# Optimization experiments

Hardware: AMD Instinct MI355X
Metric: run time of the kernel (lower is better)

Reference implementation:

```python
import jax, jax.numpy as jnp
from jax import lax
import numpy as np

B, T, D = 8, 512, 512
TS = 2 * T          # skip length = upsampled length
DI, DS, DTR, K, NL = 2 * D, 16, 32, 4, 2  # d_inner, d_state, dt_rank, d_conv, n_layers


def setup_inputs() -> dict:
    key = jax.random.key(0)
    ks = jax.random.split(key, 12)
    f = lambda k, s: jax.random.normal(k, s, dtype=jnp.float32)
    sc = 0.02
    A_log = jnp.log(jnp.arange(1, DS + 1, dtype=jnp.float32))  # S4D-real init
    A_log = jnp.tile(A_log[None, None, :], (NL, DI, 1))
    return {
        "x": f(ks[0], (B, T, D)),
        "skip": f(ks[1], (B, TS, D)),
        "up_w": f(ks[2], (D, D, K)) * sc,        # torch ConvTranspose1d weight (in,out,k)
        "up_b": jnp.zeros((D,), jnp.float32),
        "merge_w": f(ks[3], (D, 2 * D)) * sc,    # 1x1 conv (out,in)
        "merge_b": jnp.zeros((D,), jnp.float32),
        "ln_w": jnp.ones((D,), jnp.float32),
        "ln_b": jnp.zeros((D,), jnp.float32),
        "in_proj_w": f(ks[4], (NL, 2 * DI, D)) * sc,
        "conv_w": f(ks[5], (NL, DI, K)) * sc,    # depthwise causal conv
        "conv_b": jnp.zeros((NL, DI), jnp.float32),
        "x_proj_w": f(ks[6], (NL, DTR + 2 * DS, DI)) * sc,
        "dt_proj_w": f(ks[7], (NL, DI, DTR)) * sc,
        "dt_proj_b": f(ks[8], (NL, DI)) * 0.1,
        "A_log": A_log,
        "D_param": jnp.ones((NL, DI), jnp.float32),
        "out_proj_w": f(ks[9], (NL, D, DI)) * sc,
    }


def _mamba(u, iw, cw, cb, xw, dw, db, alog, dpar, ow):
    # u: (B,L,D) -> (B,L,D). Standard Mamba block (expand=2, d_state=16, d_conv=4).
    b, L, _ = u.shape
    di, ds, dtr = cw.shape[0], alog.shape[1], dw.shape[1]
    xz = jnp.einsum('bld,ed->ble', u, iw)          # (B,L,2*di)
    xi, z = jnp.split(xz, 2, axis=-1)
    # depthwise causal conv over time
    xc = lax.conv_general_dilated(xi.transpose(0, 2, 1), cw[:, None, :], (1,),
                                  [(K - 1, 0)], feature_group_count=di,
                                  dimension_numbers=('NCH', 'OIH', 'NCH')) + cb[:, None]
    xc = jax.nn.silu(xc).transpose(0, 2, 1)        # (B,L,di)
    xdbl = jnp.einsum('bld,ed->ble', xc, xw)       # (B,L,dtr+2*ds)
    dt, Bm, Cm = jnp.split(xdbl, [dtr, dtr + ds], axis=-1)
    dt = jax.nn.softplus(jnp.einsum('blr,dr->bld', dt, dw) + db)  # (B,L,di)
    A = -jnp.exp(alog)                              # (di,ds)

    def step(h, inp):
        dt_t, B_t, C_t, u_t = inp                   # (B,di),(B,ds),(B,ds),(B,di)
        h = jnp.exp(dt_t[:, :, None] * A) * h + (dt_t * u_t)[:, :, None] * B_t[:, None, :]
        return h, jnp.einsum('bds,bs->bd', h, C_t)

    h0 = jnp.zeros((b, di, ds), u.dtype)
    _, ys = lax.scan(step, h0, (dt.transpose(1, 0, 2), Bm.transpose(1, 0, 2),
                                Cm.transpose(1, 0, 2), xc.transpose(1, 0, 2)))
    y = ys.transpose(1, 0, 2) + dpar * xc           # D skip connection
    y = y * jax.nn.silu(z)                          # gating
    return jnp.einsum('bld,od->blo', y, ow)


def reference(x, skip, up_w, up_b, merge_w, merge_b, ln_w, ln_b,
              in_proj_w, conv_w, conv_b, x_proj_w, dt_proj_w, dt_proj_b,
              A_log, D_param, out_proj_w):
    # ConvTranspose1d(k=4,s=2,p=1): dilated conv with flipped, transposed kernel
    kern = jnp.flip(jnp.swapaxes(up_w, 0, 1), -1)   # (out,in,k)
    xu = lax.conv_general_dilated(x.transpose(0, 2, 1), kern, (1,), [(2, 2)],
                                  lhs_dilation=(2,),
                                  dimension_numbers=('NCH', 'OIH', 'NCH')) + up_b[:, None]
    Ts = skip.shape[1]
    xu = xu[:, :, :Ts]                              # T_up == T_skip here (2T)
    cat = jnp.concatenate([xu.transpose(0, 2, 1), skip], axis=-1)  # (B,Ts,2D)
    merged = jnp.einsum('btc,oc->bto', cat, merge_w) + merge_b     # 1x1 conv merge
    mu = merged.mean(-1, keepdims=True)
    var = merged.var(-1, keepdims=True)
    out = (merged - mu) * lax.rsqrt(var + 1e-5) * ln_w + ln_b      # LayerNorm
    for i in range(in_proj_w.shape[0]):             # stacked Mamba layers
        out = _mamba(out, in_proj_w[i], conv_w[i], conv_b[i], x_proj_w[i],
                     dt_proj_w[i], dt_proj_b[i], A_log[i], D_param[i], out_proj_w[i])
    return out
```

## Files before the change

kernel.cpp:

```cpp
#include <hip/hip_runtime.h>

#define DEV __device__ __forceinline__

typedef short  bf16x8 __attribute__((ext_vector_type(8)));
typedef float  f32x4  __attribute__((ext_vector_type(4)));

DEV unsigned short f2b(float f) {
    unsigned int u = __float_as_uint(f);
    u += 0x7fffu + ((u >> 16) & 1u);
    return (unsigned short)(u >> 16);
}
DEV float b2f(unsigned short h) { return __uint_as_float((unsigned int)h << 16); }
DEV float silu(float x) { return x / (1.f + __expf(-x)); }
DEV float fexp2(float x) { return __builtin_amdgcn_exp2f(x); }
DEV float flog2(float x) { return __builtin_amdgcn_logf(x); }

typedef const __attribute__((address_space(1))) unsigned int GU32;
typedef __attribute__((address_space(3))) unsigned int LU32;
DEV void gload16(const unsigned short* g, unsigned short* l) {
    __builtin_amdgcn_global_load_lds((GU32*)g, (LU32*)l, 16, 0, 0);
}

__global__ __launch_bounds__(256) void k_prep(
        const float* __restrict__ x, const float* __restrict__ merge_w,
        const float* __restrict__ in_proj_w, const float* __restrict__ x_proj_w,
        const float* __restrict__ out_proj_w, const float* __restrict__ dt_proj_w,
        unsigned short* __restrict__ xbf, unsigned short* __restrict__ mw,
        unsigned short* __restrict__ ipw, unsigned short* __restrict__ xpw,
        unsigned short* __restrict__ opw, unsigned short* __restrict__ dtpB) {
    size_t i = (size_t)blockIdx.x * 256 + threadIdx.x;
    const size_t n0 = 524288;
    const size_t n1 = n0 + 131072;
    const size_t n2 = n1 + 524288;
    const size_t n3 = n2 + 32768;
    const size_t n4 = n3 + 262144;
    const size_t n5 = n4 + 65536;
    if (i < n4) {
        const float* s; unsigned short* d; size_t j;
        if (i < n0)      { s = x;          d = xbf; j = i; }
        else if (i < n1) { s = merge_w;    d = mw;  j = i - n0; }
        else if (i < n2) { s = in_proj_w;  d = ipw; j = i - n1; }
        else if (i < n3) { s = x_proj_w;   d = xpw; j = i - n2; }
        else             { s = out_proj_w; d = opw; j = i - n3; }
        float4 v = *(const float4*)(s + j * 4);
        ushort4 o = { f2b(v.x), f2b(v.y), f2b(v.z), f2b(v.w) };
        *(ushort4*)(d + j * 4) = o;
    } else if (i < n5) {
        size_t j = i - n4;
        int r = (int)(j & 31);
        size_t dg = j >> 5;
        float xw = dt_proj_w[dg * 32 + r];
        unsigned short wh = f2b(xw);
        unsigned short wl = f2b(xw - b2f(wh));
        size_t base = dg * 128;
        dtpB[base + r]      = wh;
        dtpB[base + 32 + r] = wl;
        dtpB[base + 64 + r] = wl;
        dtpB[base + 96 + r] = wh;
    }
}

__global__ void k_upT(const float* __restrict__ up_w, unsigned short* __restrict__ upT) {
    __shared__ float t[32][33];
    int tx = threadIdx.x, ty = threadIdx.y;
    int o0 = blockIdx.x * 32, i0 = blockIdx.y * 32, kz = blockIdx.z;
    t[ty][tx] = up_w[(size_t)(i0 + ty) * 2048 + (o0 + tx) * 4 + kz];
    __syncthreads();
    upT[(size_t)(kz * 512 + o0 + ty) * 512 + i0 + tx] = f2b(t[tx][ty]);
}

template <int BM, int BN, int OUTMODE>
__global__ __launch_bounds__(256) void k_gemm(const unsigned short* __restrict__ A,
                                              const unsigned short* __restrict__ B,
                                              float* __restrict__ Cf,
                                              unsigned short* __restrict__ Cb,
                                              const float* __restrict__ bias,
                                              int M, int N, int K) {
    constexpr int BK = 64;
    constexpr int WM = (BN == 128) ? 64 : 32;
    constexpr int WN = (BM == 64 && BN == 64) ? 32 : 64;
    constexpr int MI = WM / 16, NI = WN / 16;
    __shared__ unsigned short As[BM * BK];
    __shared__ unsigned short Bs[BN * BK];
    const int tid = threadIdx.x;
    const int wid = tid >> 6, lane = tid & 63;

    int bid = blockIdx.y * gridDim.x + blockIdx.x;
    const int nwg = gridDim.x * gridDim.y;
    if ((nwg & 7) == 0) {
        int cpx = nwg >> 3;
        bid = (bid & 7) * cpx + (bid >> 3);
    }
    const int bx = bid % gridDim.x, by = bid / gridDim.x;
    const int m0 = by * BM, n0 = bx * BN;

    int wr, wc;
    if (BN == 128)      { wr = wid >> 1; wc = wid & 1; }
    else if (BM == 128) { wr = wid;      wc = 0;       }
    else                { wr = wid & 1;  wc = wid >> 1; }
    const int wm0 = wr * WM, wn0 = wc * WN;
    const int fr = lane & 15, fh = lane >> 4;

    const int srow = lane >> 3;
    const int scol = (((lane & 7) ^ srow)) * 8;
    const unsigned short* Ag = A + (size_t)(m0 + wid * 8 + srow) * K + scol;
    const unsigned short* Bg = B + (size_t)(n0 + wid * 8 + srow) * K + scol;
    unsigned short* AsB = &As[wid * 8 * BK];
    unsigned short* BsB = &Bs[wid * 8 * BK];

    f32x4 acc[MI][NI];
#pragma unroll
    for (int i = 0; i < MI; ++i)
#pragma unroll
        for (int j = 0; j < NI; ++j) acc[i][j] = (f32x4){0.f, 0.f, 0.f, 0.f};

    const int frx = fr & 7;
    for (int k0 = 0; k0 < K; k0 += BK) {
#pragma unroll
        for (int i = 0; i < BM / 32; ++i)
            gload16(Ag + (size_t)(i * 32) * K + k0, AsB + i * 32 * BK);
#pragma unroll
        for (int i = 0; i < BN / 32; ++i)
            gload16(Bg + (size_t)(i * 32) * K + k0, BsB + i * 32 * BK);
        __syncthreads();
#pragma unroll
        for (int kk = 0; kk < BK; kk += 32) {
            bf16x8 av[MI], bv[NI];
#pragma unroll
            for (int mi = 0; mi < MI; ++mi)
                av[mi] = *(const bf16x8*)(&As[(wm0 + mi * 16 + fr) * BK +
                                              ((((kk >> 3) + fh) ^ frx) << 3)]);
#pragma unroll
            for (int ni = 0; ni < NI; ++ni)
                bv[ni] = *(const bf16x8*)(&Bs[(wn0 + ni * 16 + fr) * BK +
                                              ((((kk >> 3) + fh) ^ frx) << 3)]);
#pragma unroll
            for (int mi = 0; mi < MI; ++mi)
#pragma unroll
                for (int ni = 0; ni < NI; ++ni)
                    acc[mi][ni] = __builtin_amdgcn_mfma_f32_16x16x32_bf16(av[mi], bv[ni],
                                                                          acc[mi][ni], 0, 0, 0);
        }
        __syncthreads();
    }
    constexpr float LOG2E = 1.4426950408889634f;
    constexpr float LN2   = 0.6931471805599453f;
#pragma unroll
    for (int mi = 0; mi < MI; ++mi) {
#pragma unroll
        for (int ni = 0; ni < NI; ++ni) {
            int col = n0 + wn0 + ni * 16 + fr;
            float bb = bias ? bias[col] : 0.f;
#pragma unroll
            for (int j = 0; j < 4; ++j) {
                int row = m0 + wm0 + mi * 16 + fh * 4 + j;
                float v = acc[mi][ni][j] + bb;
                if (OUTMODE == 0)      Cf[(size_t)row * N + col] = v;
                else if (OUTMODE == 1) Cb[(size_t)row * N + col] = f2b(v);
                else if (OUTMODE == 4) {
                    Cf[(size_t)row * N + col] = v;
                    if (col < 32) {
                        unsigned short xh = f2b(v);
                        unsigned short xl = f2b(v - b2f(xh));
                        size_t base = (size_t)row * 128;
                        Cb[base + col]      = xh;
                        Cb[base + 32 + col] = xl;
                        Cb[base + 64 + col] = xh;
                        Cb[base + 96 + col] = xl;
                    }
                } else {
                    float sp = (v > 20.f) ? v : flog2(1.f + fexp2(v * LOG2E)) * LN2;
                    if (OUTMODE == 2) Cf[(size_t)row * N + col] = sp;
                    else              Cb[(size_t)row * N + col] = f2b(sp);
                }
            }
        }
    }
}

__global__ __launch_bounds__(256) void k_assemble(const float* __restrict__ P,
                                                  const float* __restrict__ skip,
                                                  const float* __restrict__ up_b,
                                                  unsigned short* __restrict__ catbf) {
    int bx = blockIdx.x;
    int m = bx >> 2;
    int c = (bx & 3) * 256 + threadIdx.x;
    int b = m >> 10, t = m & 1023, j = t >> 1;
    float v;
    if (c < 512) {
        size_t rb = (size_t)((b << 9) + j) * 2048;
        if (t & 1) {
            v = P[rb + 1024 + c];
            if (j + 1 < 512) v += P[rb + 2048 + c];
        } else {
            v = P[rb + 512 + c];
            if (j >= 1) v += P[rb - 2048 + 1536 + c];
        }
        v += up_b[c];
    } else {
        v = skip[(size_t)m * 512 + (c - 512)];
    }
    catbf[(size_t)m * 1024 + c] = f2b(v);
}

__global__ __launch_bounds__(256) void k_ln(const float* __restrict__ merged,
                                            const float* __restrict__ w,
                                            const float* __restrict__ bvec,
                                            unsigned short* __restrict__ outb) {
    int row = blockIdx.x * 4 + (threadIdx.x >> 6);
    int lane = threadIdx.x & 63;
    const float* r = merged + (size_t)row * 512 + lane * 8;
    float4 v1 = *(const float4*)r;
    float4 v2 = *(const float4*)(r + 4);
    float xv[8] = {v1.x, v1.y, v1.z, v1.w, v2.x, v2.y, v2.z, v2.w};
    float s = 0.f, ss = 0.f;
#pragma unroll
    for (int e = 0; e < 8; ++e) { s += xv[e]; ss += xv[e] * xv[e]; }
#pragma unroll
    for (int m = 1; m < 64; m <<= 1) { s += __shfl_xor(s, m, 64); ss += __shfl_xor(ss, m, 64); }
    float mean = s * (1.f / 512.f);
    float var = ss * (1.f / 512.f) - mean * mean;
    float inv = rsqrtf(var + 1e-5f);
    unsigned short o8[8];
#pragma unroll
    for (int e = 0; e < 8; ++e) {
        int c = lane * 8 + e;
        o8[e] = f2b((xv[e] - mean) * inv * w[c] + bvec[c]);
    }
    *(int4*)(outb + (size_t)row * 512 + lane * 8) = *(const int4*)o8;
}

__global__ __launch_bounds__(256) void k_conv(const unsigned short* __restrict__ xzb,
                                              const float* __restrict__ cw,
                                              const float* __restrict__ cb,
                                              unsigned short* __restrict__ xcb) {
    int i = blockIdx.x * 256 + threadIdx.x;
    int m = i >> 8;
    int c0 = (i & 255) * 4;
    int l = m & 1023;
    float4 w0 = *(const float4*)(cw + (size_t)(c0 + 0) * 4);
    float4 w1 = *(const float4*)(cw + (size_t)(c0 + 1) * 4);
    float4 w2 = *(const float4*)(cw + (size_t)(c0 + 2) * 4);
    float4 w3 = *(const float4*)(cw + (size_t)(c0 + 3) * 4);
    float4 acc = *(const float4*)(cb + c0);
    const float* wp0 = (const float*)&w0;
    const float* wp1 = (const float*)&w1;
    const float* wp2 = (const float*)&w2;
    const float* wp3 = (const float*)&w3;
#pragma unroll
    for (int k = 0; k < 4; ++k) {
        int lp = l - 3 + k;
        if (lp >= 0) {
            ushort4 xv = *(const ushort4*)(xzb + (size_t)(m - l + lp) * 2048 + c0);
            acc.x = fmaf(wp0[k], b2f(xv.x), acc.x);
            acc.y = fmaf(wp1[k], b2f(xv.y), acc.y);
            acc.z = fmaf(wp2[k], b2f(xv.z), acc.z);
            acc.w = fmaf(wp3[k], b2f(xv.w), acc.w);
        }
    }
    ushort4 o = { f2b(silu(acc.x)), f2b(silu(acc.y)), f2b(silu(acc.z)), f2b(silu(acc.w)) };
    *(ushort4*)(xcb + (size_t)m * 1024 + c0) = o;
}

constexpr int SCAN_NC = 32;
constexpr int SCAN_CL = 32;

template <int PHASE>
__global__ __launch_bounds__(256) void k_scan_chunk(
        const unsigned short* __restrict__ dtb, const unsigned short* __restrict__ xcb,
        const float* __restrict__ xdbl, const unsigned short* __restrict__ xzb,
        const float* __restrict__ Alog, const float* __restrict__ Dp,
        unsigned int* __restrict__ sum, const unsigned short* __restrict__ hinit,
        unsigned short* __restrict__ ybf) {
    constexpr int CL = SCAN_CL;
    const int tid = threadIdx.x;
    const int d0 = blockIdx.x * 256;
    const int d = d0 + tid;
    const int b = blockIdx.y, c = blockIdx.z;
    const size_t mbase = (size_t)b * 1024 + (size_t)c * CL;

    __shared__ float sBC[CL][32];
    __shared__ unsigned short sdt[CL][256];
    __shared__ unsigned short su[CL][256];
    {
        int row = tid >> 3, q = tid & 7;
        *(float4*)&sBC[row][q * 4] =
            *(const float4*)(xdbl + (mbase + row) * 64 + 32 + q * 4);
    }
    for (int i = tid; i < CL * 32; i += 256) {
        int row = i >> 5, q = i & 31;
        const size_t g = (mbase + row) * 1024 + d0 + q * 8;
        *(int4*)&sdt[row][q * 8] = *(const int4*)(dtb + g);
        *(int4*)&su[row][q * 8]  = *(const int4*)(xcb + g);
    }
    __syncthreads();

    constexpr float LOG2E = 1.4426950408889634f;
    float A2[16], h[16];
#pragma unroll
    for (int s = 0; s < 16; ++s) A2[s] = -expf(Alog[d * 16 + s]) * LOG2E;

    bool powok = true;
#pragma unroll
    for (int s = 1; s < 16; ++s)
        powok = powok && (fabsf(A2[s] - (float)(s + 1) * A2[0]) <=
                          1e-5f * fabsf(A2[s]));

    const size_t sumbase = ((size_t)(b * SCAN_NC + c) << 14) + d * 16;
    if (PHASE == 0) {
#pragma unroll
        for (int s = 0; s < 16; ++s) h[s] = 0.f;
    } else {
#pragma unroll
        for (int s = 0; s < 16; s += 8) {
            bf16x8 hv = *(const bf16x8*)(hinit + sumbase + s);
#pragma unroll
            for (int j = 0; j < 8; ++j) h[s + j] = b2f((unsigned short)hv[j]);
        }
    }
    float dtsum = 0.f;
    const float Dv = (PHASE == 1) ? Dp[d] : 0.f;

    float zv_n = 0.f;
    if (PHASE == 1) zv_n = b2f(xzb[mbase * 2048 + 1024 + d]);

#pragma unroll 2
    for (int l = 0; l < CL; ++l) {
        const size_t m = mbase + l;
        const float dtv_c = b2f(sdt[l][tid]);
        const float uv_c  = b2f(su[l][tid]);
        float zv;
        if (PHASE == 1) {
            zv = zv_n;
            if (l + 1 < CL) zv_n = b2f(xzb[(m + 1) * 2048 + 1024 + d]);
        }
        const float dtu = dtv_c * uv_c;
        if (PHASE == 0) dtsum += dtv_c;
        float Bv[16], Cv[16];
#pragma unroll
        for (int q = 0; q < 4; ++q) {
            *(float4*)&Bv[q * 4] = *(const float4*)&sBC[l][q * 4];
            if (PHASE == 1)
                *(float4*)&Cv[q * 4] = *(const float4*)&sBC[l][16 + q * 4];
        }
        float p = 0.f;
        if (powok) {
            const float a1 = fexp2(dtv_c * A2[0]);
            float a = a1;
#pragma unroll
            for (int s = 0; s < 16; ++s) {
                h[s] = fmaf(a, h[s], dtu * Bv[s]);
                if (PHASE == 1) p = fmaf(h[s], Cv[s], p);
                a *= a1;
            }
        } else {
#pragma unroll
            for (int s = 0; s < 16; ++s) {
                float a = fexp2(dtv_c * A2[s]);
                h[s] = fmaf(a, h[s], dtu * Bv[s]);
                if (PHASE == 1) p = fmaf(h[s], Cv[s], p);
            }
        }
        if (PHASE == 1) {
            ybf[m * 1024 + d] = f2b((p + Dv * uv_c) * silu(zv));
        }
    }
    if (PHASE == 0) {
        float aprod[16];
        if (powok) {
            const float ap1 = fexp2(A2[0] * dtsum);
            float a = ap1;
#pragma unroll
            for (int s = 0; s < 16; ++s) { aprod[s] = a; a *= ap1; }
        } else {
#pragma unroll
            for (int s = 0; s < 16; ++s) aprod[s] = fexp2(A2[s] * dtsum);
        }
        unsigned int pk[16];
#pragma unroll
        for (int s = 0; s < 16; ++s)
            pk[s] = (unsigned int)f2b(aprod[s]) | ((unsigned int)f2b(h[s]) << 16);
#pragma unroll
        for (int s = 0; s < 16; s += 4)
            *(uint4*)(sum + sumbase + s) = *(const uint4*)&pk[s];
    }
}

__global__ __launch_bounds__(256) void k_scan_carry(const unsigned int* __restrict__ sum,
                                                    unsigned short* __restrict__ hinit) {
    int i = blockIdx.x * 256 + threadIdx.x;
    int b = i >> 14, ds = i & 16383;
    float h = 0.f;
    for (int c = 0; c < SCAN_NC; ++c) {
        size_t idx = ((size_t)(b * SCAN_NC + c) << 14) + ds;
        unsigned int u = sum[idx];
        float a = b2f((unsigned short)(u & 0xffffu));
        float f = b2f((unsigned short)(u >> 16));
        hinit[idx] = f2b(h);
        h = fmaf(a, h, f);
    }
}

extern "C" void kernel_launch(void* const* d_in, const int* in_sizes, int n_in,
                              void* d_out, int out_size, void* d_ws, size_t ws_size,
                              hipStream_t stream) {
    const float* x         = (const float*)d_in[0];
    const float* skip      = (const float*)d_in[1];
    const float* up_w      = (const float*)d_in[2];
    const float* up_b      = (const float*)d_in[3];
    const float* merge_w   = (const float*)d_in[4];
    const float* merge_b   = (const float*)d_in[5];
    const float* ln_w      = (const float*)d_in[6];
    const float* ln_b      = (const float*)d_in[7];
    const float* in_proj_w = (const float*)d_in[8];
    const float* conv_w    = (const float*)d_in[9];
    const float* conv_b    = (const float*)d_in[10];
    const float* x_proj_w  = (const float*)d_in[11];
    const float* dt_proj_w = (const float*)d_in[12];
    const float* dt_proj_b = (const float*)d_in[13];
    const float* A_log     = (const float*)d_in[14];
    const float* D_param   = (const float*)d_in[15];
    const float* out_proj_w= (const float*)d_in[16];
    float* out = (float*)d_out;

    char* ws = (char*)d_ws;
    size_t off = 0;
    auto alloc = [&](size_t bytes) { size_t r = off; off += (bytes + 255) & ~(size_t)255; return r; };

    unsigned short* upT  = (unsigned short*)(ws + alloc(2048ull * 512 * 2));
    unsigned short* mw   = (unsigned short*)(ws + alloc(512ull * 1024 * 2));
    unsigned short* ipw  = (unsigned short*)(ws + alloc(2ull * 2048 * 512 * 2));
    unsigned short* xpw  = (unsigned short*)(ws + alloc(2ull * 64 * 1024 * 2));
    unsigned short* opw  = (unsigned short*)(ws + alloc(2ull * 512 * 1024 * 2));
    unsigned short* xbf  = (unsigned short*)(ws + alloc(4096ull * 512 * 2));
    unsigned short* ubf  = (unsigned short*)(ws + alloc(8192ull * 512 * 2));
    unsigned short* xzbf  = (unsigned short*)(ws + alloc(8192ull * 2048 * 2));
    unsigned short* xcbf  = (unsigned short*)(ws + alloc(8192ull * 1024 * 2));
    float*          xdbl  = (float*)(ws + alloc(8192ull * 64 * 4));
    unsigned short* dtbf  = (unsigned short*)(ws + alloc(8192ull * 1024 * 2));
    unsigned short* ybf   = (unsigned short*)(ws + alloc(8192ull * 1024 * 2));
    unsigned int*   scan_sum   = (unsigned int*)(ws + alloc((size_t)SCAN_NC * 8 * 16384 * 4));
    unsigned short* scan_hinit = (unsigned short*)(ws + alloc((size_t)SCAN_NC * 8 * 16384 * 2));
    unsigned short* dtpA  = (unsigned short*)(ws + alloc(8192ull * 128 * 2));
    unsigned short* dtpB  = (unsigned short*)(ws + alloc(2048ull * 128 * 2));
    float*          P      = (float*)xzbf;
    unsigned short* catbf  = dtbf;
    float*          merged = (float*)xcbf;

    k_prep<<<6017, 256, 0, stream>>>(x, merge_w, in_proj_w, x_proj_w, out_proj_w,
                                     dt_proj_w, xbf, mw, ipw, xpw, opw, dtpB);
    k_upT<<<dim3(16, 16, 4), dim3(32, 32), 0, stream>>>(up_w, upT);

    k_gemm<128, 128, 0><<<dim3(16, 32), 256, 0, stream>>>(xbf, upT, P, nullptr, nullptr,
                                                          4096, 2048, 512);
    k_assemble<<<32768, 256, 0, stream>>>(P, skip, up_b, catbf);
    k_gemm<128, 128, 0><<<dim3(4, 64), 256, 0, stream>>>(catbf, mw, merged, nullptr, merge_b,
                                                         8192, 512, 1024);
    k_ln<<<2048, 256, 0, stream>>>(merged, ln_w, ln_b, ubf);

    for (int li = 0; li < 2; ++li) {
        k_gemm<128, 128, 1><<<dim3(16, 64), 256, 0, stream>>>(ubf, ipw + (size_t)li * 2048 * 512,
                                                              nullptr, xzbf, nullptr, 8192, 2048, 512);
        k_conv<<<8192, 256, 0, stream>>>(xzbf, conv_w + li * 4096, conv_b + li * 1024, xcbf);
        k_gemm<64, 64, 4><<<dim3(1, 128), 256, 0, stream>>>(xcbf, xpw + (size_t)li * 64 * 1024,
                                                            xdbl, dtpA, nullptr, 8192, 64, 1024);
        k_gemm<128, 64, 3><<<dim3(16, 64), 256, 0, stream>>>(dtpA, dtpB + (size_t)li * 1024 * 128,
                                                             nullptr, dtbf,
                                                             dt_proj_b + (size_t)li * 1024,
                                                             8192, 1024, 128);
        const float* Al = A_log + (size_t)li * 1024 * 16;
        const float* Dl = D_param + (size_t)li * 1024;
        k_scan_chunk<0><<<dim3(4, 8, SCAN_NC), 256, 0, stream>>>(
            dtbf, xcbf, xdbl, xzbf, Al, Dl, scan_sum, scan_hinit, ybf);
        k_scan_carry<<<512, 256, 0, stream>>>(scan_sum, scan_hinit);
        k_scan_chunk<1><<<dim3(4, 8, SCAN_NC), 256, 0, stream>>>(
            dtbf, xcbf, xdbl, xzbf, Al, Dl, scan_sum, scan_hinit, ybf);
        if (li == 0)
            k_gemm<128, 128, 1><<<dim3(4, 64), 256, 0, stream>>>(ybf, opw, nullptr, ubf, nullptr,
                                                                 8192, 512, 1024);
        else
            k_gemm<128, 128, 0><<<dim3(4, 64), 256, 0, stream>>>(ybf, opw + (size_t)512 * 1024,
                                                                 out, nullptr, nullptr, 8192, 512, 1024);
    }
}
```

Before: 408.4 us.

## Precompute scan A table in prep and store upsample GEMM output as bf16

Moves the per-thread computation of A = -exp(A_log)*log2e and the power-series check out of the scan kernels. They are now computed once in the prep kernel and stored as a table plus a per-channel flag. Separately, the transposed-conv GEMM now writes bf16 instead of fp32, which halves the P traffic read by the assemble kernel. The bf16 intermediate costs some precision on the upsampled values before they are summed.

```diff
diff --git a/kernel.cpp b/kernel.cpp
--- a/kernel.cpp
+++ b/kernel.cpp
@@ -25,9 +25,11 @@
         const float* __restrict__ x, const float* __restrict__ merge_w,
         const float* __restrict__ in_proj_w, const float* __restrict__ x_proj_w,
         const float* __restrict__ out_proj_w, const float* __restrict__ dt_proj_w,
+        const float* __restrict__ A_log,
         unsigned short* __restrict__ xbf, unsigned short* __restrict__ mw,
         unsigned short* __restrict__ ipw, unsigned short* __restrict__ xpw,
-        unsigned short* __restrict__ opw, unsigned short* __restrict__ dtpB) {
+        unsigned short* __restrict__ opw, unsigned short* __restrict__ dtpB,
+        float* __restrict__ A2tab, int* __restrict__ powflag) {
     size_t i = (size_t)blockIdx.x * 256 + threadIdx.x;
     const size_t n0 = 524288;
     const size_t n1 = n0 + 131072;
@@ -35,6 +37,7 @@
     const size_t n3 = n2 + 32768;
     const size_t n4 = n3 + 262144;
     const size_t n5 = n4 + 65536;
+    const size_t n6 = n5 + 2048;
     if (i < n4) {
         const float* s; unsigned short* d; size_t j;
         if (i < n0)      { s = x;          d = xbf; j = i; }
@@ -57,6 +60,21 @@
         dtpB[base + 32 + r] = wl;
         dtpB[base + 64 + r] = wl;
         dtpB[base + 96 + r] = wh;
+    } else if (i < n6) {
+        size_t dg = i - n5;
+        constexpr float LOG2E = 1.4426950408889634f;
+        float a2[16];
+#pragma unroll
+        for (int s = 0; s < 16; ++s)
+            a2[s] = -expf(A_log[dg * 16 + s]) * LOG2E;
+        bool ok = true;
+#pragma unroll
+        for (int s = 1; s < 16; ++s)
+            ok = ok && (fabsf(a2[s] - (float)(s + 1) * a2[0]) <= 1e-5f * fabsf(a2[s]));
+#pragma unroll
+        for (int s = 0; s < 16; s += 4)
+            *(f32x4*)(A2tab + dg * 16 + s) = *(const f32x4*)&a2[s];
+        powflag[dg] = ok ? 1 : 0;
     }
 }
 
@@ -178,7 +196,7 @@
     }
 }
 
-__global__ __launch_bounds__(256) void k_assemble(const float* __restrict__ P,
+__global__ __launch_bounds__(256) void k_assemble(const unsigned short* __restrict__ P,
                                                   const float* __restrict__ skip,
                                                   const float* __restrict__ up_b,
                                                   unsigned short* __restrict__ catbf) {
@@ -190,11 +208,11 @@
     if (c < 512) {
         size_t rb = (size_t)((b << 9) + j) * 2048;
         if (t & 1) {
-            v = P[rb + 1024 + c];
-            if (j + 1 < 512) v += P[rb + 2048 + c];
+            v = b2f(P[rb + 1024 + c]);
+            if (j + 1 < 512) v += b2f(P[rb + 2048 + c]);
         } else {
-            v = P[rb + 512 + c];
-            if (j >= 1) v += P[rb - 2048 + 1536 + c];
+            v = b2f(P[rb + 512 + c]);
+            if (j >= 1) v += b2f(P[rb - 2048 + 1536 + c]);
         }
         v += up_b[c];
     } else {
@@ -269,7 +287,8 @@
 __global__ __launch_bounds__(256) void k_scan_chunk(
         const unsigned short* __restrict__ dtb, const unsigned short* __restrict__ xcb,
         const float* __restrict__ xdbl, const unsigned short* __restrict__ xzb,
-        const float* __restrict__ Alog, const float* __restrict__ Dp,
+        const float* __restrict__ A2tab, const int* __restrict__ powflag,
+        const float* __restrict__ Dp,
         unsigned int* __restrict__ sum, const unsigned short* __restrict__ hinit,
         unsigned short* __restrict__ ybf) {
     constexpr int CL = SCAN_CL;
@@ -295,16 +314,11 @@
     }
     __syncthreads();
 
-    constexpr float LOG2E = 1.4426950408889634f;
     float A2[16], h[16];
 #pragma unroll
-    for (int s = 0; s < 16; ++s) A2[s] = -expf(Alog[d * 16 + s]) * LOG2E;
-
-    bool powok = true;
-#pragma unroll
-    for (int s = 1; s < 16; ++s)
-        powok = powok && (fabsf(A2[s] - (float)(s + 1) * A2[0]) <=
-                          1e-5f * fabsf(A2[s]));
+    for (int s = 0; s < 16; s += 4)
+        *(f32x4*)&A2[s] = *(const f32x4*)(A2tab + (size_t)d * 16 + s);
+    const bool powok = powflag[d] != 0;
 
     const size_t sumbase = ((size_t)(b * SCAN_NC + c) << 14) + d * 16;
     if (PHASE == 0) {
@@ -434,6 +448,8 @@
     unsigned short* opw  = (unsigned short*)(ws + alloc(2ull * 512 * 1024 * 2));
     unsigned short* xbf  = (unsigned short*)(ws + alloc(4096ull * 512 * 2));
     unsigned short* ubf  = (unsigned short*)(ws + alloc(8192ull * 512 * 2));
+    float*          A2tab   = (float*)(ws + alloc(2048ull * 16 * 4));
+    int*            powflag = (int*)(ws + alloc(2048ull * 4));
     unsigned short* xzbf  = (unsigned short*)(ws + alloc(8192ull * 2048 * 2));
     unsigned short* xcbf  = (unsigned short*)(ws + alloc(8192ull * 1024 * 2));
     float*          xdbl  = (float*)(ws + alloc(8192ull * 64 * 4));
@@ -443,15 +459,16 @@
     unsigned short* scan_hinit = (unsigned short*)(ws + alloc((size_t)SCAN_NC * 8 * 16384 * 2));
     unsigned short* dtpA  = (unsigned short*)(ws + alloc(8192ull * 128 * 2));
     unsigned short* dtpB  = (unsigned short*)(ws + alloc(2048ull * 128 * 2));
-    float*          P      = (float*)xzbf;
+    unsigned short* P      = xzbf;
     unsigned short* catbf  = dtbf;
     float*          merged = (float*)xcbf;
 
-    k_prep<<<6017, 256, 0, stream>>>(x, merge_w, in_proj_w, x_proj_w, out_proj_w,
-                                     dt_proj_w, xbf, mw, ipw, xpw, opw, dtpB);
+    k_prep<<<6024, 256, 0, stream>>>(x, merge_w, in_proj_w, x_proj_w, out_proj_w,
+                                     dt_proj_w, A_log, xbf, mw, ipw, xpw, opw, dtpB,
+                                     A2tab, powflag);
     k_upT<<<dim3(16, 16, 4), dim3(32, 32), 0, stream>>>(up_w, upT);
 
-    k_gemm<128, 128, 0><<<dim3(16, 32), 256, 0, stream>>>(xbf, upT, P, nullptr, nullptr,
+    k_gemm<128, 128, 1><<<dim3(16, 32), 256, 0, stream>>>(xbf, upT, nullptr, P, nullptr,
                                                           4096, 2048, 512);
     k_assemble<<<32768, 256, 0, stream>>>(P, skip, up_b, catbf);
     k_gemm<128, 128, 0><<<dim3(4, 64), 256, 0, stream>>>(catbf, mw, merged, nullptr, merge_b,
@@ -468,13 +485,14 @@
                                                              nullptr, dtbf,
                                                              dt_proj_b + (size_t)li * 1024,
                                                              8192, 1024, 128);
-        const float* Al = A_log + (size_t)li * 1024 * 16;
-        const float* Dl = D_param + (size_t)li * 1024;
+        const float* A2l = A2tab + (size_t)li * 1024 * 16;
+        const int*   pfl = powflag + (size_t)li * 1024;
+        const float* Dl  = D_param + (size_t)li * 1024;
         k_scan_chunk<0><<<dim3(4, 8, SCAN_NC), 256, 0, stream>>>(
-            dtbf, xcbf, xdbl, xzbf, Al, Dl, scan_sum, scan_hinit, ybf);
+            dtbf, xcbf, xdbl, xzbf, A2l, pfl, Dl, scan_sum, scan_hinit, ybf);
         k_scan_carry<<<512, 256, 0, stream>>>(scan_sum, scan_hinit);
         k_scan_chunk<1><<<dim3(4, 8, SCAN_NC), 256, 0, stream>>>(
-            dtbf, xcbf, xdbl, xzbf, Al, Dl, scan_sum, scan_hinit, ybf);
+            dtbf, xcbf, xdbl, xzbf, A2l, pfl, Dl, scan_sum, scan_hinit, ybf);
         if (li == 0)
             k_gemm<128, 128, 1><<<dim3(4, 64), 256, 0, stream>>>(ybf, opw, nullptr, ubf, nullptr,
                                                                  8192, 512, 1024);
```

Result: no change. 404.4 us (-1.0%).
